# Kernel optimization log

Hardware: AMD Instinct MI355X
Metric: run time of the kernel (lower is better)

The kernel has to match this reference:

```python
import jax, jax.numpy as jnp
import numpy as np

B, S, F = 4, 2048, 1024

def setup_inputs() -> dict:
    key = jax.random.key(0)
    ks = jax.random.split(key, 9)
    s = 1.0 / np.sqrt(F)
    return {
        "q": jax.random.normal(ks[0], (B, S, F), jnp.float32),
        "k": jax.random.normal(ks[1], (B, S, F), jnp.float32),
        "v": jax.random.normal(ks[2], (B, S, F), jnp.float32),
        "Wq": jax.random.normal(ks[3], (F, F), jnp.float32) * s,
        "bq": jax.random.normal(ks[4], (F,), jnp.float32) * s,
        "Wk": jax.random.normal(ks[5], (F, F), jnp.float32) * s,
        "bk": jax.random.normal(ks[6], (F,), jnp.float32) * s,
        "Wv": jax.random.normal(ks[7], (F, F), jnp.float32) * s,
        "bv": jax.random.normal(ks[8], (F,), jnp.float32) * s,
    }

def reference(q, k, v, Wq, bq, Wk, bk, Wv, bv):
    # Linear layers: x @ W^T + b (torch nn.Linear convention)
    qp = jnp.einsum('bsf,gf->bsg', q, Wq) + bq
    kp = jnp.einsum('bsf,gf->bsg', k, Wk) + bk
    vp = jnp.einsum('bsf,gf->bsg', v, Wv) + bv
    # Unscaled attention (no 1/sqrt(d)), as in the original module
    attn = jax.nn.softmax(jnp.einsum('bqf,bkf->bqk', qp, kp), axis=-1)
    return jnp.einsum('bqk,bkf->bqf', attn, vp) + q
```

## Files before the change

kernel.cpp:

```cpp
#include <hip/hip_runtime.h>

typedef unsigned short u16;
typedef __bf16 bf16x8 __attribute__((ext_vector_type(8)));
typedef float f32x4 __attribute__((ext_vector_type(4)));
typedef u16 u16x8 __attribute__((ext_vector_type(8)));

union B8 { u16x8 u; bf16x8 b; };

__device__ __forceinline__ u16 f2b(float f){
  unsigned u = __float_as_uint(f);
  return (u16)((u + 0x7FFFu + ((u >> 16) & 1u)) >> 16);
}
__device__ __forceinline__ float b2f(u16 h){ return __uint_as_float(((unsigned)h) << 16); }

__device__ __forceinline__ void gload16(const u16* g, u16* l){
  __builtin_amdgcn_global_load_lds((const __attribute__((address_space(1))) void*)g,
                                   (__attribute__((address_space(3))) void*)l, 16, 0, 0);
}

__global__ __launch_bounds__(256) void prep_kernel(
    const float* __restrict__ v, const float* __restrict__ Wv,
    const float* __restrict__ Wq, const float* __restrict__ Wk,
    u16* __restrict__ v_b, u16* __restrict__ Wv_b,
    u16* __restrict__ WqT_pair, u16* __restrict__ WkT_pair)
{
  __shared__ float lds[64][65];
  const int blk = blockIdx.x, t = threadIdx.x;
  if (blk < 4608){
    const float* src; u16* dst; long base;
    if (blk < 4096){ src = v;  dst = v_b;  base = blk; }
    else           { src = Wv; dst = Wv_b; base = blk - 4096; }
    long i = base * 256 + t;
    float4 x0 = ((const float4*)src)[2 * i];
    float4 x1 = ((const float4*)src)[2 * i + 1];
    float xs[8] = {x0.x, x0.y, x0.z, x0.w, x1.x, x1.y, x1.z, x1.w};
    u16x8 h;
    #pragma unroll
    for (int j = 0; j < 8; j++) h[j] = f2b(xs[j]);
    ((u16x8*)dst)[i] = h;
  } else {
    int tt = blk - 4608;
    const float* W = (tt >> 8) ? Wk : Wq;
    u16* outp      = (tt >> 8) ? WkT_pair : WqT_pair;
    int t16 = tt & 255, g0 = (t16 >> 4) * 64, f0 = (t16 & 15) * 64;
    int c4 = (t & 15) * 4, r0 = t >> 4;
    #pragma unroll
    for (int it = 0; it < 4; it++){
      int r = r0 + it * 16;
      float4 x = *(const float4*)&W[(long)(g0 + r) * 1024 + f0 + c4];
      lds[r][c4] = x.x; lds[r][c4+1] = x.y; lds[r][c4+2] = x.z; lds[r][c4+3] = x.w;
    }
    __syncthreads();
    #pragma unroll
    for (int it = 0; it < 2; it++){
      int task = t + it * 256;
      int fl = task >> 3, gi = task & 7;
      u16x8 h, l;
      #pragma unroll
      for (int jj = 0; jj < 8; jj++){
        float xv = lds[gi * 8 + jj][fl];
        h[jj] = f2b(xv); l[jj] = f2b(xv - b2f(h[jj]));
      }
      u16* o = outp + (long)(f0 + fl) * 2048 + ((g0 >> 3) + gi) * 16;
      *(u16x8*)o = h;
      *(u16x8*)(o + 8) = l;
    }
  }
}

__global__ __launch_bounds__(256) void bvec_kernel(
    const u16* __restrict__ WkT_pair, const float* __restrict__ bq, float* __restrict__ b)
{
  const int wave = threadIdx.x >> 6, lane = threadIdx.x & 63;
  const int e = blockIdx.x * 4 + wave;
  const u16* row = WkT_pair + (long)e * 2048;
  float acc = 0.f;
  #pragma unroll
  for (int ii = 0; ii < 2; ii++){
    int gi = lane * 2 + ii;
    const u16* p = row + gi * 16;
    #pragma unroll
    for (int j = 0; j < 8; j++)
      acc += (b2f(p[j]) + b2f(p[j + 8])) * bq[gi * 8 + j];
  }
  #pragma unroll
  for (int off = 32; off > 0; off >>= 1) acc += __shfl_xor(acc, off, 64);
  if (lane == 0) b[e] = acc;
}

__global__ __launch_bounds__(256) void split_qk_kernel(
    const float* __restrict__ q, const float* __restrict__ kk,
    const float* __restrict__ b,
    u16* __restrict__ q_pair, u16* __restrict__ k_pair, float* __restrict__ kb)
{
  const int blk = blockIdx.x, t = threadIdx.x;
  const bool isK = blk >= 4096;
  const float* src = isK ? kk : q;
  u16* dst = isK ? k_pair : q_pair;
  long base = isK ? blk - 4096 : blk;
  long i = base * 256 + t;
  float4 x0 = ((const float4*)src)[2 * i];
  float4 x1 = ((const float4*)src)[2 * i + 1];
  float xs[8] = {x0.x, x0.y, x0.z, x0.w, x1.x, x1.y, x1.z, x1.w};
  u16x8 h, l;
  #pragma unroll
  for (int j = 0; j < 8; j++){ h[j] = f2b(xs[j]); l[j] = f2b(xs[j] - b2f(h[j])); }
  ((u16x8*)dst)[2 * i]     = h;
  ((u16x8*)dst)[2 * i + 1] = l;
  if (isK){
    const int f = (t & 127) * 8;
    float d = 0.f;
    #pragma unroll
    for (int j = 0; j < 8; j++) d += xs[j] * b[f + j];
    #pragma unroll
    for (int off = 32; off > 0; off >>= 1) d += __shfl_xor(d, off, 64);
    __shared__ float red[4];
    if ((t & 63) == 0) red[t >> 6] = d;
    __syncthreads();
    if (t == 0)   kb[base * 2]     = red[0] + red[1];
    if (t == 128) kb[base * 2 + 1] = red[2] + red[3];
  }
}

__global__ __launch_bounds__(256) void reduce_split_kernel(
    const float* __restrict__ part, u16* __restrict__ out_pair, long nper)
{
  long i = (long)blockIdx.x * 256 + threadIdx.x;
  float s[8];
  #pragma unroll
  for (int j = 0; j < 8; j++) s[j] = 0.f;
  #pragma unroll
  for (int z = 0; z < 4; z++){
    float4 a0 = ((const float4*)(part + z * nper))[2 * i];
    float4 a1 = ((const float4*)(part + z * nper))[2 * i + 1];
    s[0]+=a0.x; s[1]+=a0.y; s[2]+=a0.z; s[3]+=a0.w;
    s[4]+=a1.x; s[5]+=a1.y; s[6]+=a1.z; s[7]+=a1.w;
  }
  u16x8 h, l;
  #pragma unroll
  for (int j = 0; j < 8; j++){ h[j] = f2b(s[j]); l[j] = f2b(s[j] - b2f(h[j])); }
  long e = (i * 8) >> 10;
  long g = i & 127;
  u16* o = out_pair + e * 2048 + g * 16;
  *(u16x8*)o = h;
  *(u16x8*)(o + 8) = l;
}

__device__ __forceinline__ void xcd_remap(int& tx, int& ty, int& tz){
  const int GX = gridDim.x, GY = gridDim.y;
  int b  = blockIdx.x + GX * (blockIdx.y + GY * blockIdx.z);
  int NB = GX * GY * gridDim.z;
  int rank = (b & 7) * (NB >> 3) + (b >> 3);
  int pz = GX * GY;
  tz = rank / pz;
  int r = rank - tz * pz;
  ty = r / GX;
  tx = r - ty * GX;
}

constexpr int BM = 128, BN = 128, BK = 32;

__device__ __forceinline__ int lds1_idx(int row, int g){ return row * 32 + g * 8; }
__device__ __forceinline__ int lds2_idx(int row, int g){
  return row * 64 + (((g ^ (row & 7)) & 7) << 3);
}

template<bool DUAL, int EPI>
__device__ __forceinline__ void gemm_nt_body(
    int tx, int ty, int tz, u16* __restrict__ lds0, u16* __restrict__ lds1,
    const u16* __restrict__ A, const u16* __restrict__ Bm,
    const float* __restrict__ bias, const float* __restrict__ residual,
    void* __restrict__ out0,
    int M, int N, int K, int Krow,
    long sAb, long sBb, long sOb, long sRb, int seq)
{
  const int t = threadIdx.x;
  const int tileM = ty * BM;
  const int tileN = tx * BN;
  const long rs = DUAL ? 2L * Krow : (long)Krow;

  const u16* gA = A  + tz * sAb + (long)tileM * rs;
  const u16* gB = Bm + tz * sBb + (long)tileN * rs;

  const int wave = t >> 6, lane = t & 63;
  const int wm = (wave >> 1) * 64, wn = (wave & 1) * 64;
  const int lr = lane & 15;
  const int lg = lane >> 4;

  const u16 *pa, *pb;
  long jstride;
  int  ldsbase, ldsstep, nissue, kadv;
  if (DUAL){
    const int lr8 = lane >> 3, sl = lane & 7;
    const int g = sl ^ lr8;
    pa = gA + (long)(wave * 32 + lr8) * rs + g * 8;
    pb = gB + (long)(wave * 32 + lr8) * rs + g * 8;
    jstride = 8 * rs;
    ldsbase = (wave * 32) * 64; ldsstep = 8 * 64;
    nissue = 4; kadv = 64;
  } else {
    pa = gA + (long)(wave * 32 + (lane >> 2)) * rs + (lane & 3) * 8;
    pb = gB + (long)(wave * 32 + (lane >> 2)) * rs + (lane & 3) * 8;
    jstride = 16 * rs;
    ldsbase = (wave * 32) * 32; ldsstep = 16 * 32;
    nissue = 2; kadv = 32;
  }

  f32x4 acc[4][4] = {};

  for (int k0 = 0; k0 < K; k0 += BK){
    __syncthreads();
    #pragma unroll 4
    for (int j = 0; j < nissue; j++){
      gload16(pa + j * jstride, &lds0[ldsbase + j * ldsstep]);
      gload16(pb + j * jstride, &lds1[ldsbase + j * ldsstep]);
    }
    pa += kadv; pb += kadv;
    __syncthreads();

    if (DUAL){
      B8 ah[4], al[4], bh[4], bl[4];
      #pragma unroll
      for (int mt = 0; mt < 4; mt++){
        int row = wm + mt * 16 + lr;
        ah[mt].u = *(const u16x8*)&lds0[lds2_idx(row, lg * 2)];
        al[mt].u = *(const u16x8*)&lds0[lds2_idx(row, lg * 2 + 1)];
      }
      #pragma unroll
      for (int nt = 0; nt < 4; nt++){
        int row = wn + nt * 16 + lr;
        bh[nt].u = *(const u16x8*)&lds1[lds2_idx(row, lg * 2)];
        bl[nt].u = *(const u16x8*)&lds1[lds2_idx(row, lg * 2 + 1)];
      }
      #pragma unroll
      for (int mt = 0; mt < 4; mt++){
        #pragma unroll
        for (int nt = 0; nt < 4; nt++){
          acc[mt][nt] = __builtin_amdgcn_mfma_f32_16x16x32_bf16(ah[mt].b, bh[nt].b, acc[mt][nt], 0, 0, 0);
          acc[mt][nt] = __builtin_amdgcn_mfma_f32_16x16x32_bf16(ah[mt].b, bl[nt].b, acc[mt][nt], 0, 0, 0);
          acc[mt][nt] = __builtin_amdgcn_mfma_f32_16x16x32_bf16(al[mt].b, bh[nt].b, acc[mt][nt], 0, 0, 0);
        }
      }
    } else {
      B8 af[4], bf[4];
      #pragma unroll
      for (int mt = 0; mt < 4; mt++)
        af[mt].u = *(const u16x8*)&lds0[lds1_idx(wm + mt * 16 + lr, lg)];
      #pragma unroll
      for (int nt = 0; nt < 4; nt++)
        bf[nt].u = *(const u16x8*)&lds1[lds1_idx(wn + nt * 16 + lr, lg)];
      #pragma unroll
      for (int mt = 0; mt < 4; mt++)
        #pragma unroll
        for (int nt = 0; nt < 4; nt++)
          acc[mt][nt] = __builtin_amdgcn_mfma_f32_16x16x32_bf16(af[mt].b, bf[nt].b, acc[mt][nt], 0, 0, 0);
    }
  }

  const int rq = lg * 4;
  #pragma unroll
  for (int nt = 0; nt < 4; nt++){
    const int n = tileN + wn + nt * 16 + lr;
    float bv = 0.f;
    if (EPI == 0 && bias) bv = bias[n];
    if (EPI == 2 && bias) bv = bias[(long)tz * N + n];
    #pragma unroll
    for (int mt = 0; mt < 4; mt++){
      #pragma unroll
      for (int r = 0; r < 4; r++){
        const int m = tileM + wm + mt * 16 + rq + r;
        float val = acc[mt][nt][r] + bv;
        if (EPI == 0){
          u16 h = f2b(val);
          u16* o = (u16*)out0 + (long)tz * sOb + (long)m * 2 * N + ((n >> 3) << 4) + (n & 7);
          o[0] = h;
          o[8] = f2b(val - b2f(h));
        } else if (EPI == 2){
          ((float*)out0)[(long)tz * sOb + (long)m * N + n] = val;
        } else if (EPI == 3){
          float res = residual[(long)tz * sRb + (long)m * N + n];
          ((float*)out0)[(long)tz * sOb + (long)m * N + n] = val + res;
        } else {
          if (bias) val += bias[m];
          long idx = (long)(n / seq) * ((long)M * seq) + (long)m * seq + (n % seq);
          ((u16*)out0)[idx] = f2b(val);
        }
      }
    }
  }
}

template<bool DUAL, int EPI>
__global__ __launch_bounds__(256, 4)
void gemm_nt(const u16* __restrict__ A, const u16* __restrict__ Bm,
             const float* __restrict__ bias, const float* __restrict__ residual,
             void* __restrict__ out0,
             int M, int N, int K, int Krow,
             long sAb, long sBb, long sOb, long sRb, int seq)
{
  constexpr int RW = DUAL ? 64 : 32;
  __shared__ u16 sh[2 * BM * RW];
  int tx, ty, tz; xcd_remap(tx, ty, tz);
  gemm_nt_body<DUAL, EPI>(tx, ty, tz, sh, sh + BM * RW,
                          A, Bm, bias, residual, out0,
                          M, N, K, Krow, sAb, sBb, sOb, sRb, seq);
}

__global__ __launch_bounds__(256, 4)
void gemm_step37(const u16* __restrict__ Wv_b, const u16* __restrict__ v_b,
                 const float* __restrict__ bv, u16* __restrict__ vpT,
                 const u16* __restrict__ q_pair, const u16* __restrict__ Mt_pair,
                 u16* __restrict__ tmp_pair)
{
  __shared__ u16 sh[2 * BM * 64];
  const int b = blockIdx.x, xcd = b & 7, i = b >> 3;
  if (i < 64){
    const int rank = xcd * 64 + i;
    gemm_nt_body<false, 4>(rank & 63, rank >> 6, 0, sh, sh + BM * 32,
                           Wv_b, v_b, bv, nullptr, vpT,
                           1024, 8192, 1024, 1024, 0, 0, 0, 0, 2048);
  } else {
    const int rank = xcd * 64 + (i - 64);
    gemm_nt_body<true, 0>(rank & 7, rank >> 3, 0, sh, sh + BM * 64,
                          q_pair, Mt_pair, nullptr, nullptr, tmp_pair,
                          8192, 1024, 1024, 1024, 0, 0, 0, 0, 2048);
  }
}

__global__ __launch_bounds__(256)
void softmax_kernel(const float* __restrict__ S, u16* __restrict__ P, int n){
  const long row = blockIdx.x;
  const float* r = S + row * (long)n;
  const int t = threadIdx.x;
  float v[8];
  float mx = -3.0e38f;
  #pragma unroll
  for (int i = 0; i < 8; i++){ v[i] = r[t + (i << 8)]; mx = fmaxf(mx, v[i]); }
  #pragma unroll
  for (int off = 32; off > 0; off >>= 1) mx = fmaxf(mx, __shfl_xor(mx, off, 64));
  __shared__ float red[8];
  const int wave = t >> 6;
  if ((t & 63) == 0) red[wave] = mx;
  __syncthreads();
  mx = fmaxf(fmaxf(red[0], red[1]), fmaxf(red[2], red[3]));
  float s = 0.f;
  #pragma unroll
  for (int i = 0; i < 8; i++){ v[i] = __expf(v[i] - mx); s += v[i]; }
  #pragma unroll
  for (int off = 32; off > 0; off >>= 1) s += __shfl_xor(s, off, 64);
  if ((t & 63) == 0) red[4 + wave] = s;
  __syncthreads();
  s = red[4] + red[5] + red[6] + red[7];
  const float inv = 1.f / s;
  u16* pr = P + row * (long)n;
  #pragma unroll
  for (int i = 0; i < 8; i++) pr[t + (i << 8)] = f2b(v[i] * inv);
}

extern "C" void kernel_launch(void* const* d_in, const int* in_sizes, int n_in,
                              void* d_out, int out_size, void* d_ws, size_t ws_size,
                              hipStream_t stream){
  (void)in_sizes; (void)n_in; (void)out_size; (void)ws_size;
  const float* q  = (const float*)d_in[0];
  const float* k  = (const float*)d_in[1];
  const float* v  = (const float*)d_in[2];
  const float* Wq = (const float*)d_in[3];
  const float* bq = (const float*)d_in[4];
  const float* Wk = (const float*)d_in[5];
  const float* Wv = (const float*)d_in[7];
  const float* bv = (const float*)d_in[8];
  float* out = (float*)d_out;

  const int B = 4, S = 2048, F = 1024;
  const long NSF = (long)B * S * F;
  const long NFF = (long)F * F;
  const long NSS = (long)B * S * S;

  char* w = (char*)d_ws;
  auto alloc = [&](long bytes) -> char* {
    char* p = w; w += (bytes + 255) & ~(long)255; return p;
  };
  u16*   tmp_pair = (u16*)alloc(2 * NSF * 2);
  u16*   k_pair   = (u16*)alloc(2 * NSF * 2);
  u16*   vpT      = (u16*)alloc(NSF * 2);
  float* kb       = (float*)alloc((long)B * S * 4);
  char* zone2 = alloc(NSS * 2 + NSS * 4);
  u16*   attn   = (u16*)zone2;
  float* scores = (float*)(zone2 + NSS * 2);
  u16*   q_pair   = (u16*)zone2;
  char*  z3       = zone2 + NSS * 2;
  u16*   v_b      = (u16*)z3;
  u16*   Wv_b     = (u16*)(z3 + NSF * 2);
  u16*   WqT_pair = (u16*)(z3 + NSF * 2 + NFF * 2);
  u16*   WkT_pair = WqT_pair + 2 * NFF;
  float* b_vec    = (float*)(WkT_pair + 2 * NFF);
  float* Mt_part  = (float*)((char*)b_vec + 4096);
  u16*   Mt_pair  = (u16*)((char*)Mt_part + 4 * NFF * 4);

  dim3 blk(256);

  prep_kernel<<<dim3(5120), blk, 0, stream>>>(
      v, Wv, Wq, Wk, v_b, Wv_b, WqT_pair, WkT_pair);

  bvec_kernel<<<dim3(256), blk, 0, stream>>>(WkT_pair, bq, b_vec);

  split_qk_kernel<<<dim3(8192), blk, 0, stream>>>(q, k, b_vec, q_pair, k_pair, kb);

  gemm_nt<true, 2><<<dim3(F / BN, F / BM, 4), blk, 0, stream>>>(
      WkT_pair, WqT_pair, nullptr, nullptr, Mt_part,
      F, F, 256, F, 512, 512, NFF, 0, S);

  reduce_split_kernel<<<dim3(512), blk, 0, stream>>>(Mt_part, Mt_pair, NFF);

  gemm_step37<<<dim3(1024), blk, 0, stream>>>(
      Wv_b, v_b, bv, vpT, q_pair, Mt_pair, tmp_pair);

  gemm_nt<true, 2><<<dim3(S / BN, S / BM, B), blk, 0, stream>>>(
      tmp_pair, k_pair, kb, nullptr, scores,
      S, S, F, F, (long)S * 2 * F, (long)S * 2 * F, (long)S * S, 0, S);

  softmax_kernel<<<dim3(B * S), blk, 0, stream>>>(scores, attn, S);

  gemm_nt<false, 3><<<dim3(F / BN, S / BM, B), blk, 0, stream>>>(
      attn, vpT, nullptr, q, out,
      S, F, S, S, (long)S * S, (long)F * S, (long)S * F, (long)S * F, S);
}
```

Before: 422.3 us.

## Fold bias-vector compute into prep and fuse Mt GEMM with q/k split

The bias-vector kernel is removed: four extra blocks in the prep kernel compute Wk^T·bq directly from the fp32 weights. The split-K Mt GEMM and the q/k bf16 hi/lo splitting kernel are merged into one launch, with GEMM blocks placed first and splitting blocks after. This cuts two kernel launches and lets the small GEMM overlap with the bandwidth-bound split work. The four b_vec blocks each loop serially over 1024 rows, so they may become a long tail inside the prep kernel.

Result: slower. 455.5 us (+7.9%).

```diff
diff --git a/kernel.cpp b/kernel.cpp
--- a/kernel.cpp
+++ b/kernel.cpp
@@ -21,15 +21,27 @@
 __global__ __launch_bounds__(256) void prep_kernel(
     const float* __restrict__ v, const float* __restrict__ Wv,
     const float* __restrict__ Wq, const float* __restrict__ Wk,
+    const float* __restrict__ bq,
     u16* __restrict__ v_b, u16* __restrict__ Wv_b,
-    u16* __restrict__ WqT_pair, u16* __restrict__ WkT_pair)
+    u16* __restrict__ WqT_pair, u16* __restrict__ WkT_pair,
+    float* __restrict__ b_vec)
 {
   __shared__ float lds[64][65];
   const int blk = blockIdx.x, t = threadIdx.x;
-  if (blk < 4608){
+  if (blk < 4){
+    const int e = blk * 256 + t;
+    float acc = 0.f;
+    #pragma unroll 8
+    for (int g = 0; g < 1024; g++)
+      acc += Wk[(long)g * 1024 + e] * bq[g];
+    b_vec[e] = acc;
+    return;
+  }
+  const int b2 = blk - 4;
+  if (b2 < 4608){
     const float* src; u16* dst; long base;
-    if (blk < 4096){ src = v;  dst = v_b;  base = blk; }
-    else           { src = Wv; dst = Wv_b; base = blk - 4096; }
+    if (b2 < 4096){ src = v;  dst = v_b;  base = b2; }
+    else          { src = Wv; dst = Wv_b; base = b2 - 4096; }
     long i = base * 256 + t;
     float4 x0 = ((const float4*)src)[2 * i];
     float4 x1 = ((const float4*)src)[2 * i + 1];
@@ -39,7 +51,7 @@
     for (int j = 0; j < 8; j++) h[j] = f2b(xs[j]);
     ((u16x8*)dst)[i] = h;
   } else {
-    int tt = blk - 4608;
+    int tt = b2 - 4608;
     const float* W = (tt >> 8) ? Wk : Wq;
     u16* outp      = (tt >> 8) ? WkT_pair : WqT_pair;
     int t16 = tt & 255, g0 = (t16 >> 4) * 64, f0 = (t16 & 15) * 64;
@@ -65,60 +77,6 @@
       *(u16x8*)o = h;
       *(u16x8*)(o + 8) = l;
     }
-  }
-}
-
-__global__ __launch_bounds__(256) void bvec_kernel(
-    const u16* __restrict__ WkT_pair, const float* __restrict__ bq, float* __restrict__ b)
-{
-  const int wave = threadIdx.x >> 6, lane = threadIdx.x & 63;
-  const int e = blockIdx.x * 4 + wave;
-  const u16* row = WkT_pair + (long)e * 2048;
-  float acc = 0.f;
-  #pragma unroll
-  for (int ii = 0; ii < 2; ii++){
-    int gi = lane * 2 + ii;
-    const u16* p = row + gi * 16;
-    #pragma unroll
-    for (int j = 0; j < 8; j++)
-      acc += (b2f(p[j]) + b2f(p[j + 8])) * bq[gi * 8 + j];
-  }
-  #pragma unroll
-  for (int off = 32; off > 0; off >>= 1) acc += __shfl_xor(acc, off, 64);
-  if (lane == 0) b[e] = acc;
-}
-
-__global__ __launch_bounds__(256) void split_qk_kernel(
-    const float* __restrict__ q, const float* __restrict__ kk,
-    const float* __restrict__ b,
-    u16* __restrict__ q_pair, u16* __restrict__ k_pair, float* __restrict__ kb)
-{
-  const int blk = blockIdx.x, t = threadIdx.x;
-  const bool isK = blk >= 4096;
-  const float* src = isK ? kk : q;
-  u16* dst = isK ? k_pair : q_pair;
-  long base = isK ? blk - 4096 : blk;
-  long i = base * 256 + t;
-  float4 x0 = ((const float4*)src)[2 * i];
-  float4 x1 = ((const float4*)src)[2 * i + 1];
-  float xs[8] = {x0.x, x0.y, x0.z, x0.w, x1.x, x1.y, x1.z, x1.w};
-  u16x8 h, l;
-  #pragma unroll
-  for (int j = 0; j < 8; j++){ h[j] = f2b(xs[j]); l[j] = f2b(xs[j] - b2f(h[j])); }
-  ((u16x8*)dst)[2 * i]     = h;
-  ((u16x8*)dst)[2 * i + 1] = l;
-  if (isK){
-    const int f = (t & 127) * 8;
-    float d = 0.f;
-    #pragma unroll
-    for (int j = 0; j < 8; j++) d += xs[j] * b[f + j];
-    #pragma unroll
-    for (int off = 32; off > 0; off >>= 1) d += __shfl_xor(d, off, 64);
-    __shared__ float red[4];
-    if ((t & 63) == 0) red[t >> 6] = d;
-    __syncthreads();
-    if (t == 0)   kb[base * 2]     = red[0] + red[1];
-    if (t == 128) kb[base * 2 + 1] = red[2] + red[3];
   }
 }
 
@@ -307,6 +265,53 @@
 }
 
 __global__ __launch_bounds__(256, 4)
+void fused_s5_qk(const u16* __restrict__ WkT_pair, const u16* __restrict__ WqT_pair,
+                 float* __restrict__ Mt_part,
+                 const float* __restrict__ q, const float* __restrict__ kk,
+                 const float* __restrict__ b,
+                 u16* __restrict__ q_pair, u16* __restrict__ k_pair,
+                 float* __restrict__ kb)
+{
+  __shared__ u16 sh[2 * BM * 64];
+  const int blk = blockIdx.x, t = threadIdx.x;
+  if (blk < 256){
+    const int rank = (blk & 7) * 32 + (blk >> 3);
+    const int tz = rank >> 6, rem = rank & 63;
+    gemm_nt_body<true, 2>(rem & 7, rem >> 3, tz, sh, sh + BM * 64,
+                          WkT_pair, WqT_pair, nullptr, nullptr, Mt_part,
+                          1024, 1024, 256, 1024, 512, 512, 1024L * 1024, 0, 2048);
+    return;
+  }
+  const int sblk = blk - 256;
+  const bool isK = sblk >= 4096;
+  const float* src = isK ? kk : q;
+  u16* dst = isK ? k_pair : q_pair;
+  long base = isK ? sblk - 4096 : sblk;
+  long i = base * 256 + t;
+  float4 x0 = ((const float4*)src)[2 * i];
+  float4 x1 = ((const float4*)src)[2 * i + 1];
+  float xs[8] = {x0.x, x0.y, x0.z, x0.w, x1.x, x1.y, x1.z, x1.w};
+  u16x8 h, l;
+  #pragma unroll
+  for (int j = 0; j < 8; j++){ h[j] = f2b(xs[j]); l[j] = f2b(xs[j] - b2f(h[j])); }
+  ((u16x8*)dst)[2 * i]     = h;
+  ((u16x8*)dst)[2 * i + 1] = l;
+  if (isK){
+    const int f = (t & 127) * 8;
+    float d = 0.f;
+    #pragma unroll
+    for (int j = 0; j < 8; j++) d += xs[j] * b[f + j];
+    #pragma unroll
+    for (int off = 32; off > 0; off >>= 1) d += __shfl_xor(d, off, 64);
+    float* red = (float*)sh;
+    if ((t & 63) == 0) red[t >> 6] = d;
+    __syncthreads();
+    if (t == 0)   kb[base * 2]     = red[0] + red[1];
+    if (t == 128) kb[base * 2 + 1] = red[2] + red[3];
+  }
+}
+
+__global__ __launch_bounds__(256, 4)
 void gemm_step37(const u16* __restrict__ Wv_b, const u16* __restrict__ v_b,
                  const float* __restrict__ bv, u16* __restrict__ vpT,
                  const u16* __restrict__ q_pair, const u16* __restrict__ Mt_pair,
@@ -399,16 +404,11 @@
 
   dim3 blk(256);
 
-  prep_kernel<<<dim3(5120), blk, 0, stream>>>(
-      v, Wv, Wq, Wk, v_b, Wv_b, WqT_pair, WkT_pair);
-
-  bvec_kernel<<<dim3(256), blk, 0, stream>>>(WkT_pair, bq, b_vec);
-
-  split_qk_kernel<<<dim3(8192), blk, 0, stream>>>(q, k, b_vec, q_pair, k_pair, kb);
-
-  gemm_nt<true, 2><<<dim3(F / BN, F / BM, 4), blk, 0, stream>>>(
-      WkT_pair, WqT_pair, nullptr, nullptr, Mt_part,
-      F, F, 256, F, 512, 512, NFF, 0, S);
+  prep_kernel<<<dim3(5124), blk, 0, stream>>>(
+      v, Wv, Wq, Wk, bq, v_b, Wv_b, WqT_pair, WkT_pair, b_vec);
+
+  fused_s5_qk<<<dim3(8448), blk, 0, stream>>>(
+      WkT_pair, WqT_pair, Mt_part, q, k, b_vec, q_pair, k_pair, kb);
 
   reduce_split_kernel<<<dim3(512), blk, 0, stream>>>(Mt_part, Mt_pair, NFF);
 
```
